# Optimization experiments

Measured on AMD Instinct MI355X. Metric: run time of the kernel, lower is better.

The kernel has to match this reference:

```python
import jax, jax.numpy as jnp
import numpy as np

B, S, D, H = 2, 2048, 1024, 16
DH = D // H
CBS, STRIDE = 32, 16      # compress block size / sliding stride
NSEL = 16                 # num_selected_blocks
WIN = 16                  # sliding_window_size (half-width)
SCALE = DH ** -0.5


def setup_inputs() -> dict:
    key = jax.random.key(0)
    ks = jax.random.split(key, 12)
    s = 0.02
    return {
        "x": jax.random.normal(ks[0], (B, S, D), jnp.float32),
        "qkv_w": jax.random.normal(ks[1], (D, 3 * D), jnp.float32) * s,
        "qkv_b": jnp.zeros((3 * D,), jnp.float32),
        "c1_w": jax.random.normal(ks[2], (CBS * D, D), jnp.float32) * s,
        "c1_b": jnp.zeros((D,), jnp.float32),
        "c2_w": jax.random.normal(ks[3], (D, D), jnp.float32) * s,
        "c2_b": jnp.zeros((D,), jnp.float32),
        "score_w": jax.random.normal(ks[4], (D, 1), jnp.float32) * s,
        "score_b": jnp.zeros((1,), jnp.float32),
        "out_w": jax.random.normal(ks[5], (D, D), jnp.float32) * s,
        "out_b": jnp.zeros((D,), jnp.float32),
    }


def reference(x, qkv_w, qkv_b, c1_w, c1_b, c2_w, c2_b, score_w, score_b, out_w, out_b):
    # q, k, v: [B, H, S, DH]
    qkv = (x @ qkv_w + qkv_b).reshape(B, S, 3, H, DH).transpose(2, 0, 3, 1, 4)
    q, k, v = qkv[0], qkv[1], qkv[2]

    # --- token compression: overlapping blocks -> MLP ---
    starts = jnp.arange(0, S - CBS + 1, STRIDE)                 # [nb]
    blk_idx = starts[:, None] + jnp.arange(CBS)[None, :]        # [nb, CBS]
    blocks = x[:, blk_idx, :].reshape(B, starts.shape[0], CBS * D)
    hidden = jax.nn.relu(blocks @ c1_w + c1_b)
    compressed = hidden @ c2_w + c2_b                           # [B, nb, D]

    # --- block selection via learned scores + top-k ---
    scores = (compressed @ score_w + score_b)[..., 0]           # [B, nb]
    _, top_idx = jax.lax.top_k(scores, NSEL)                    # [B, NSEL]
    selected = jnp.take_along_axis(compressed, top_idx[:, :, None], axis=1)  # [B, NSEL, D]

    sqkv = (selected @ qkv_w + qkv_b).reshape(B, NSEL, 3, H, DH).transpose(2, 0, 3, 1, 4)
    sel_k, sel_v = sqkv[1], sqkv[2]                             # [B, H, NSEL, DH]

    # --- sliding-window local attention (vectorized gather of banded K/V) ---
    offs = jnp.arange(-WIN, WIN + 1)                            # [2W+1]
    pos = jnp.arange(S)[:, None] + offs[None, :]                # [S, 2W+1]
    valid = (pos >= 0) & (pos < S)
    pos_c = jnp.clip(pos, 0, S - 1)
    kw = k[:, :, pos_c, :]                                      # [B, H, S, 2W+1, DH]
    vw = v[:, :, pos_c, :]
    sc = jnp.einsum('bhsd,bhswd->bhsw', q, kw) * SCALE
    sc = jnp.where(valid[None, None], sc, -jnp.inf)
    local = jnp.einsum('bhsw,bhswd->bhsd', jax.nn.softmax(sc, axis=-1), vw)

    # --- global attention over selected compressed blocks ---
    gsc = jnp.einsum('bhsd,bhkd->bhsk', q, sel_k) * SCALE       # [B, H, S, NSEL]
    glob = jnp.einsum('bhsk,bhkd->bhsd', jax.nn.softmax(gsc, axis=-1), sel_v)

    out = (local + glob).transpose(0, 2, 1, 3).reshape(B, S, D)
    return out @ out_w + out_b
```

## Files before the change

kernel.cpp:

```cpp
#include <hip/hip_runtime.h>
#include <math.h>

#define BB   2
#define SS   2048
#define DD   1024
#define HH   16
#define DH   64
#define CBS  32
#define STRIDEC 16
#define NBLK 127
#define NSEL 16
#define WIN  16
#define NW   33
#define SCALE 0.125f
#define MC   254

typedef _Float16 f16;
typedef __attribute__((ext_vector_type(8))) _Float16 f16x8;
typedef __attribute__((ext_vector_type(4))) _Float16 f16x4;
typedef __attribute__((ext_vector_type(2))) _Float16 h2;
typedef __attribute__((ext_vector_type(4))) float f32x4;

__global__ __launch_bounds__(256) void convert_f16(
    const float* __restrict__ src, f16* __restrict__ dst, int n)
{
    const int i = (blockIdx.x * 256 + threadIdx.x) * 4;
    if (i >= n) return;
    float4 v = *(const float4*)(src + i);
    f16x4 o;
    o[0] = (f16)v.x; o[1] = (f16)v.y; o[2] = (f16)v.z; o[3] = (f16)v.w;
    *(f16x4*)(dst + i) = o;
}

__global__ __launch_bounds__(256) void transpose_conv(
    const float* __restrict__ src, f16* __restrict__ dst, int K, int N)
{
    __shared__ float t[32][33];
    const int n0 = blockIdx.x * 32, k0 = blockIdx.y * 32;
    const int tx = threadIdx.x & 31, ty = threadIdx.x >> 5;
#pragma unroll
    for (int r = 0; r < 32; r += 8)
        t[ty + r][tx] = src[(size_t)(k0 + ty + r) * N + n0 + tx];
    __syncthreads();
#pragma unroll
    for (int r = 0; r < 32; r += 8)
        dst[(size_t)(n0 + ty + r) * K + k0 + tx] = (f16)t[tx][ty + r];
}

template<int OUT16>
__global__ __launch_bounds__(256) void gemm_f16(
    const f16* __restrict__ A, const f16* __restrict__ Bt,
    const float* __restrict__ bias, float* __restrict__ C,
    int M, int N, int K)
{
    constexpr int BK = 64;
    __shared__ f16 As[128 * BK];
    __shared__ f16 Bs[128 * BK];
    const int tid  = threadIdx.x;
    const int wid  = tid >> 6, lane = tid & 63;
    const int bm = blockIdx.y * 128, bn = blockIdx.x * 128;
    const int wm = (wid >> 1) * 64, wn = (wid & 1) * 64;

    const int lrow = lane >> 3;
    const int lk8  = (lane & 7) * 8;

    f32x4 acc[4][4];
#pragma unroll
    for (int i = 0; i < 4; ++i)
#pragma unroll
        for (int j = 0; j < 4; ++j) acc[i][j] = (f32x4){0.f, 0.f, 0.f, 0.f};

    for (int kt = 0; kt < K; kt += BK) {
#pragma unroll
        for (int c = 0; c < 4; ++c) {
            const int seg = c * 4 + wid;
            const int row = seg * 8 + lrow;
            const f16* ga = A + (size_t)(bm + row) * K + kt + lk8;
            __builtin_amdgcn_global_load_lds(
                (const __attribute__((address_space(1))) void*)(const void*)ga,
                (__attribute__((address_space(3))) void*)(void*)(As + seg * 512),
                16, 0, 0);
            const f16* gb = Bt + (size_t)(bn + row) * K + kt + lk8;
            __builtin_amdgcn_global_load_lds(
                (const __attribute__((address_space(1))) void*)(const void*)gb,
                (__attribute__((address_space(3))) void*)(void*)(Bs + seg * 512),
                16, 0, 0);
        }
        __syncthreads();

#pragma unroll
        for (int kk = 0; kk < 2; ++kk) {
            const int ko = kk * 32 + (lane >> 4) * 8;
            f16x8 a[4], b[4];
#pragma unroll
            for (int i = 0; i < 4; ++i)
                a[i] = *(const f16x8*)(As + (wm + i * 16 + (lane & 15)) * BK + ko);
#pragma unroll
            for (int j = 0; j < 4; ++j)
                b[j] = *(const f16x8*)(Bs + (wn + j * 16 + (lane & 15)) * BK + ko);
#pragma unroll
            for (int i = 0; i < 4; ++i)
#pragma unroll
                for (int j = 0; j < 4; ++j)
                    acc[i][j] = __builtin_amdgcn_mfma_f32_16x16x32_f16(
                        a[i], b[j], acc[i][j], 0, 0, 0);
        }
        __syncthreads();
    }

    const int rr0 = (lane >> 4) * 4;
    const int cc  = lane & 15;
#pragma unroll
    for (int i = 0; i < 4; ++i) {
        const int r = bm + wm + i * 16 + rr0;
#pragma unroll
        for (int j = 0; j < 4; ++j) {
            const int cn = bn + wn + j * 16 + cc;
            const float bv = bias[cn];
#pragma unroll
            for (int q = 0; q < 4; ++q) {
                if constexpr (OUT16)
                    ((f16*)C)[(size_t)(r + q) * N + cn] = (f16)(acc[i][j][q] + bv);
                else
                    C[(size_t)(r + q) * N + cn] = acc[i][j][q] + bv;
            }
        }
    }
}

#define C1_NZ 16
#define C1_KCHUNK 2048

__global__ __launch_bounds__(256) void gemm_c1(
    const f16* __restrict__ xh, const float* __restrict__ c1w,
    float* __restrict__ P)
{
    constexpr int BK = 64;
    constexpr int BSTR = 72;
    __shared__ f16 As[128 * BK];
    __shared__ f16 Bs[64 * BSTR];
    const int tid  = threadIdx.x;
    const int wid  = tid >> 6, lane = tid & 63;
    const int bn = blockIdx.x * 64, bm = blockIdx.y * 128;
    const int z  = blockIdx.z;
    const int wm = (wid >> 1) * 64, wn = (wid & 1) * 32;

    const int lrow = lane >> 3;
    const int lk8  = (lane & 7) * 8;

    f32x4 acc[4][2];
#pragma unroll
    for (int i = 0; i < 4; ++i)
#pragma unroll
        for (int j = 0; j < 2; ++j) acc[i][j] = (f32x4){0.f, 0.f, 0.f, 0.f};

    for (int t = 0; t < C1_KCHUNK / BK; ++t) {
        const int ktg = z * C1_KCHUNK + t * BK;
        const int kc  = (ktg + lk8) >> 10;
        const int kd  = (ktg + lk8) & 1023;
#pragma unroll
        for (int c = 0; c < 4; ++c) {
            const int seg = c * 4 + wid;
            int row = bm + seg * 8 + lrow;
            if (row > MC - 1) row = MC - 1;
            const int b   = (row >= NBLK) ? 1 : 0;
            const int blk = row - b * NBLK;
            const f16* ga = xh + ((size_t)(b * SS + blk * STRIDEC + kc) << 10) + kd;
            __builtin_amdgcn_global_load_lds(
                (const __attribute__((address_space(1))) void*)(const void*)ga,
                (__attribute__((address_space(3))) void*)(void*)(As + seg * 512),
                16, 0, 0);
        }
        {
            const int kk0 = (tid >> 4) * 2;
            const int n4  = (tid & 15) * 4;
#pragma unroll
            for (int p = 0; p < 2; ++p) {
                const int kk = kk0 + p * 32;
                const float* gB = c1w + (size_t)(ktg + kk) * DD + bn + n4;
                float4 r0 = *(const float4*)gB;
                float4 r1 = *(const float4*)(gB + DD);
                const float a0[4] = {r0.x, r0.y, r0.z, r0.w};
                const float a1[4] = {r1.x, r1.y, r1.z, r1.w};
#pragma unroll
                for (int u = 0; u < 4; ++u) {
                    const int n = n4 + u;
                    h2 w; w[0] = (f16)a0[u]; w[1] = (f16)a1[u];
                    *(h2*)&Bs[n * BSTR + (kk ^ (((n >> 3) & 3) << 3))] = w;
                }
            }
        }
        __syncthreads();

#pragma unroll
        for (int kk = 0; kk < 2; ++kk) {
            const int ko = kk * 32 + (lane >> 4) * 8;
            f16x8 a[4], b[2];
#pragma unroll
            for (int i = 0; i < 4; ++i)
                a[i] = *(const f16x8*)(As + (wm + i * 16 + (lane & 15)) * BK + ko);
#pragma unroll
            for (int j = 0; j < 2; ++j) {
                const int n = wn + j * 16 + (lane & 15);
                b[j] = *(const f16x8*)&Bs[n * BSTR + (ko ^ (((n >> 3) & 3) << 3))];
            }
#pragma unroll
            for (int i = 0; i < 4; ++i)
#pragma unroll
                for (int j = 0; j < 2; ++j)
                    acc[i][j] = __builtin_amdgcn_mfma_f32_16x16x32_f16(
                        a[i], b[j], acc[i][j], 0, 0, 0);
        }
        __syncthreads();
    }

    const int rr0 = (lane >> 4) * 4;
    const int cc  = lane & 15;
#pragma unroll
    for (int i = 0; i < 4; ++i) {
        const int r = bm + wm + i * 16 + rr0;
#pragma unroll
        for (int j = 0; j < 2; ++j) {
            const int cn = bn + wn + j * 16 + cc;
#pragma unroll
            for (int q = 0; q < 4; ++q)
                if (r + q < MC)
                    P[((size_t)z * MC + r + q) * DD + cn] = acc[i][j][q];
        }
    }
}

template<int MODE>
__global__ __launch_bounds__(256) void gemm128(
    const float* __restrict__ A, const float* __restrict__ Bm,
    const float* __restrict__ bias, float* __restrict__ C,
    int M, int N, int K, const int* __restrict__ selIdx, int flags)
{
    __shared__ float As[8][132];
    __shared__ float Bs[8][132];

    const int tid = threadIdx.x;
    const int bm = blockIdx.y * 128;
    const int bn = blockIdx.x * 128;
    const int nz = gridDim.z;
    const int z  = blockIdx.z;
    const int kchunk = K / nz;
    const int k0 = z * kchunk;
    const int kend = k0 + kchunk;

    const int tx = tid & 15;
    const int ty = tid >> 4;

    const int arow = tid >> 1;
    const int akq  = (tid & 1) * 4;
    const int bkr  = tid >> 5;
    const int bcol = (tid & 31) * 4;

    float acc[2][2][4][4];
#pragma unroll
    for (int qi = 0; qi < 2; ++qi)
#pragma unroll
        for (int qj = 0; qj < 2; ++qj)
#pragma unroll
            for (int i = 0; i < 4; ++i)
#pragma unroll
                for (int j = 0; j < 4; ++j) acc[qi][qj][i][j] = 0.f;

    auto loadA = [&](int kt) -> float4 {
        float4 av = make_float4(0.f, 0.f, 0.f, 0.f);
        const int grow = bm + arow;
        if (grow < M) {
            if constexpr (MODE == 0) {
                av = *(const float4*)(A + (size_t)grow * K + kt + akq);
            } else {
                const int b = grow >> 4;
                const int j = grow & 15;
                const int idx = selIdx[b * NSEL + j];
                av = *(const float4*)(A + (size_t)(b * NBLK + idx) * K + kt + akq);
            }
        }
        return av;
    };
    auto loadB = [&](int kt) -> float4 {
        return *(const float4*)(Bm + (size_t)(kt + bkr) * N + bn + bcol);
    };

    float4 av = loadA(k0);
    float4 bv = loadB(k0);

    for (int kt = k0; kt < kend; kt += 8) {
        As[akq + 0][arow] = av.x;
        As[akq + 1][arow] = av.y;
        As[akq + 2][arow] = av.z;
        As[akq + 3][arow] = av.w;
        *(float4*)&Bs[bkr][bcol] = bv;
        __syncthreads();
        if (kt + 8 < kend) {
            av = loadA(kt + 8);
            bv = loadB(kt + 8);
        }
#pragma unroll
        for (int k = 0; k < 8; ++k) {
            const float4 a0 = *(const float4*)&As[k][ty * 4];
            const float4 a1 = *(const float4*)&As[k][64 + ty * 4];
            const float4 b0 = *(const float4*)&Bs[k][tx * 4];
            const float4 b1 = *(const float4*)&Bs[k][64 + tx * 4];
            const float ar[2][4] = {{a0.x, a0.y, a0.z, a0.w},
                                    {a1.x, a1.y, a1.z, a1.w}};
            const float br[2][4] = {{b0.x, b0.y, b0.z, b0.w},
                                    {b1.x, b1.y, b1.z, b1.w}};
#pragma unroll
            for (int qi = 0; qi < 2; ++qi)
#pragma unroll
                for (int i = 0; i < 4; ++i)
#pragma unroll
                    for (int qj = 0; qj < 2; ++qj)
#pragma unroll
                        for (int j = 0; j < 4; ++j)
                            acc[qi][qj][i][j] += ar[qi][i] * br[qj][j];
        }
        __syncthreads();
    }

    if (nz == 1) {
        const bool hasB   = (flags & 1) != 0;
        const bool doRelu = (flags & 2) != 0;
#pragma unroll
        for (int qi = 0; qi < 2; ++qi)
#pragma unroll
            for (int i = 0; i < 4; ++i) {
                const int r = bm + qi * 64 + ty * 4 + i;
                if (r >= M) continue;
#pragma unroll
                for (int qj = 0; qj < 2; ++qj)
#pragma unroll
                    for (int j = 0; j < 4; ++j) {
                        const int cn = bn + qj * 64 + tx * 4 + j;
                        float v = acc[qi][qj][i][j];
                        if (hasB) v += bias[cn];
                        if (doRelu) v = fmaxf(v, 0.f);
                        C[(size_t)r * N + cn] = v;
                    }
            }
    } else {
        float* P = C + (size_t)z * M * N;
#pragma unroll
        for (int qi = 0; qi < 2; ++qi)
#pragma unroll
            for (int i = 0; i < 4; ++i) {
                const int r = bm + qi * 64 + ty * 4 + i;
                if (r >= M) continue;
#pragma unroll
                for (int qj = 0; qj < 2; ++qj)
#pragma unroll
                    for (int j = 0; j < 4; ++j) {
                        const int cn = bn + qj * 64 + tx * 4 + j;
                        P[(size_t)r * N + cn] = acc[qi][qj][i][j];
                    }
            }
    }
}

__global__ __launch_bounds__(256) void reduce_partials(
    const float* __restrict__ P, const float* __restrict__ bias,
    float* __restrict__ outp, int MN, int N, int nz, int doRelu, int halfOut)
{
    const int i = blockIdx.x * 256 + threadIdx.x;
    if (i >= MN) return;
    float s = 0.f;
    for (int z = 0; z < nz; ++z) s += P[(size_t)z * MN + i];
    s += bias[i % N];
    if (doRelu) s = fmaxf(s, 0.f);
    if (halfOut) ((f16*)outp)[i] = (f16)s;
    else         outp[i] = s;
}

__global__ __launch_bounds__(256) void score_kernel(
    const float* __restrict__ comp, const float* __restrict__ sw,
    const float* __restrict__ sb, float* __restrict__ scores)
{
    const int row = blockIdx.x;
    const float* cp = comp + (size_t)row * DD;
    float s = 0.f;
    for (int k = threadIdx.x; k < DD; k += 256) s += cp[k] * sw[k];
#pragma unroll
    for (int off = 32; off >= 1; off >>= 1) s += __shfl_xor(s, off);
    __shared__ float red[4];
    if ((threadIdx.x & 63) == 0) red[threadIdx.x >> 6] = s;
    __syncthreads();
    if (threadIdx.x == 0) scores[row] = red[0] + red[1] + red[2] + red[3] + sb[0];
}

__global__ __launch_bounds__(128) void topk_kernel(
    const float* __restrict__ scores, int* __restrict__ top)
{
    const int b = blockIdx.x;
    const int t = threadIdx.x;
    __shared__ float sval[128];
    __shared__ float sv2[128];
    __shared__ int   si2[128];
    __shared__ unsigned char used[128];
    sval[t] = (t < NBLK) ? scores[b * NBLK + t] : -INFINITY;
    used[t] = 0;
    __syncthreads();
    for (int j = 0; j < NSEL; ++j) {
        sv2[t] = used[t] ? -INFINITY : sval[t];
        si2[t] = t;
        __syncthreads();
        for (int stp = 64; stp >= 1; stp >>= 1) {
            if (t < stp) {
                if (sv2[t + stp] > sv2[t] ||
                    (sv2[t + stp] == sv2[t] && si2[t + stp] < si2[t])) {
                    sv2[t] = sv2[t + stp];
                    si2[t] = si2[t + stp];
                }
            }
            __syncthreads();
        }
        if (t == 0) { top[b * NSEL + j] = si2[0]; used[si2[0]] = 1; }
        __syncthreads();
    }
}

#define QT 64
#define KROWS 96
#define KST2 72
#define VST 136
#define PST 136

__global__ __launch_bounds__(256) void attn_mfma(
    const f16* __restrict__ qkv, const f16* __restrict__ sqkv,
    f16* __restrict__ attn)
{
    __shared__ f16 Kl[KROWS][KST2];
    __shared__ f16 sKl[NSEL][KST2];
    __shared__ f16 Vt[DH][VST];
    __shared__ f16 Pl[4][16][PST];

    int bid = blockIdx.x;
    bid = (bid & 7) * (gridDim.x >> 3) + (bid >> 3);
    const int t = bid & 31;
    const int h = (bid >> 5) & (HH - 1);
    const int b = bid >> 9;
    const int s0 = t * QT;

    const int tid = threadIdx.x;
    const int wid = tid >> 6, lane = tid & 63;
    const int l15 = lane & 15, lg = lane >> 4;

    for (int i = tid; i < KROWS * 8; i += 256) {
        const int row = i >> 3, c8 = (i & 7) * 8;
        const int pos = s0 - WIN + row;
        f16x8 kv, vv;
#pragma unroll
        for (int u = 0; u < 8; ++u) { kv[u] = (f16)0.f; vv[u] = (f16)0.f; }
        if (pos >= 0 && pos < SS) {
            const f16* base = qkv + (size_t)(b * SS + pos) * (3 * DD) + h * DH + c8;
            kv = *(const f16x8*)(base + DD);
            vv = *(const f16x8*)(base + 2 * DD);
        }
        *(f16x8*)&Kl[row][c8] = kv;
#pragma unroll
        for (int u = 0; u < 8; ++u) Vt[c8 + u][row] = vv[u];
    }
    if (tid < NSEL * 8) {
        const int si = tid >> 3, c8 = (tid & 7) * 8;
        const f16* base = sqkv + (size_t)(b * NSEL + si) * (3 * DD) + h * DH + c8;
        f16x8 kv = *(const f16x8*)(base + DD);
        f16x8 vv = *(const f16x8*)(base + 2 * DD);
        *(f16x8*)&sKl[si][c8] = kv;
#pragma unroll
        for (int u = 0; u < 8; ++u) Vt[c8 + u][96 + si] = vv[u];
    }
    for (int i = tid; i < DH * 16; i += 256)
        Vt[i >> 4][112 + (i & 15)] = (f16)0.f;

    f16x8 qf[2];
    {
        const f16* qp = qkv + (size_t)(b * SS + s0 + wid * 16 + l15) * (3 * DD)
                      + h * DH + lg * 8;
        qf[0] = *(const f16x8*)(qp);
        qf[1] = *(const f16x8*)(qp + 32);
    }
    __syncthreads();

    f32x4 aqk[6], asel;
#pragma unroll
    for (int i = 0; i < 6; ++i) aqk[i] = (f32x4){0.f, 0.f, 0.f, 0.f};
    asel = (f32x4){0.f, 0.f, 0.f, 0.f};
#pragma unroll
    for (int kc = 0; kc < 2; ++kc) {
        const int ko = kc * 32 + lg * 8;
#pragma unroll
        for (int kvb = 0; kvb < 6; ++kvb) {
            f16x8 ka = *(const f16x8*)&Kl[kvb * 16 + l15][ko];
            aqk[kvb] = __builtin_amdgcn_mfma_f32_16x16x32_f16(ka, qf[kc], aqk[kvb], 0, 0, 0);
        }
        f16x8 ks = *(const f16x8*)&sKl[l15][ko];
        asel = __builtin_amdgcn_mfma_f32_16x16x32_f16(ks, qf[kc], asel, 0, 0, 0);
    }

    const int qt_ = wid * 16 + l15;
    float sc[6][4];
    float m = -INFINITY;
#pragma unroll
    for (int kvb = 0; kvb < 6; ++kvb)
#pragma unroll
        for (int r = 0; r < 4; ++r) {
            const int kv  = kvb * 16 + lg * 4 + r;
            const int pos = s0 - WIN + kv;
            const int dlt = kv - qt_;
            const bool ok = (dlt >= 0) & (dlt <= 32) & (pos >= 0) & (pos < SS);
            sc[kvb][r] = ok ? aqk[kvb][r] * SCALE : -INFINITY;
            m = fmaxf(m, sc[kvb][r]);
        }
    m = fmaxf(m, __shfl_xor(m, 16));
    m = fmaxf(m, __shfl_xor(m, 32));
    float sum = 0.f;
#pragma unroll
    for (int kvb = 0; kvb < 6; ++kvb)
#pragma unroll
        for (int r = 0; r < 4; ++r) {
            sc[kvb][r] = __expf(sc[kvb][r] - m);
            sum += sc[kvb][r];
        }
    sum += __shfl_xor(sum, 16);
    sum += __shfl_xor(sum, 32);
    const float inv1 = 1.f / sum;

    float s2[4];
    float m2 = -INFINITY;
#pragma unroll
    for (int r = 0; r < 4; ++r) { s2[r] = asel[r] * SCALE; m2 = fmaxf(m2, s2[r]); }
    m2 = fmaxf(m2, __shfl_xor(m2, 16));
    m2 = fmaxf(m2, __shfl_xor(m2, 32));
    float sum2 = 0.f;
#pragma unroll
    for (int r = 0; r < 4; ++r) { s2[r] = __expf(s2[r] - m2); sum2 += s2[r]; }
    sum2 += __shfl_xor(sum2, 16);
    sum2 += __shfl_xor(sum2, 32);
    const float inv2 = 1.f / sum2;

#pragma unroll
    for (int kvb = 0; kvb < 6; ++kvb) {
        h2 p01, p23;
        p01[0] = (f16)(sc[kvb][0] * inv1); p01[1] = (f16)(sc[kvb][1] * inv1);
        p23[0] = (f16)(sc[kvb][2] * inv1); p23[1] = (f16)(sc[kvb][3] * inv1);
        *(h2*)&Pl[wid][l15][kvb * 16 + lg * 4]     = p01;
        *(h2*)&Pl[wid][l15][kvb * 16 + lg * 4 + 2] = p23;
    }
    {
        h2 g01, g23, z0;
        g01[0] = (f16)(s2[0] * inv2); g01[1] = (f16)(s2[1] * inv2);
        g23[0] = (f16)(s2[2] * inv2); g23[1] = (f16)(s2[3] * inv2);
        z0[0] = (f16)0.f; z0[1] = (f16)0.f;
        *(h2*)&Pl[wid][l15][96 + lg * 4]      = g01;
        *(h2*)&Pl[wid][l15][96 + lg * 4 + 2]  = g23;
        *(h2*)&Pl[wid][l15][112 + lg * 4]     = z0;
        *(h2*)&Pl[wid][l15][112 + lg * 4 + 2] = z0;
    }

    f32x4 ov[4];
#pragma unroll
    for (int i = 0; i < 4; ++i) ov[i] = (f32x4){0.f, 0.f, 0.f, 0.f};
#pragma unroll
    for (int kc = 0; kc < 4; ++kc) {
        const int ko = kc * 32 + lg * 8;
        f16x8 pa = *(const f16x8*)&Pl[wid][l15][ko];
#pragma unroll
        for (int db = 0; db < 4; ++db) {
            f16x8 vb = *(const f16x8*)&Vt[db * 16 + l15][ko];
            ov[db] = __builtin_amdgcn_mfma_f32_16x16x32_f16(pa, vb, ov[db], 0, 0, 0);
        }
    }

    const size_t rbase = (size_t)(b * SS + s0 + wid * 16 + lg * 4);
#pragma unroll
    for (int r = 0; r < 4; ++r) {
        f16* op = attn + (rbase + r) * DD + h * DH + l15;
#pragma unroll
        for (int db = 0; db < 4; ++db)
            op[db * 16] = (f16)ov[db][r];
    }
}

extern "C" void kernel_launch(void* const* d_in, const int* in_sizes, int n_in,
                              void* d_out, int out_size, void* d_ws, size_t ws_size,
                              hipStream_t stream)
{
    const float* x       = (const float*)d_in[0];
    const float* qkv_w   = (const float*)d_in[1];
    const float* qkv_b   = (const float*)d_in[2];
    const float* c1_w    = (const float*)d_in[3];
    const float* c1_b    = (const float*)d_in[4];
    const float* c2_w    = (const float*)d_in[5];
    const float* c2_b    = (const float*)d_in[6];
    const float* score_w = (const float*)d_in[7];
    const float* score_b = (const float*)d_in[8];
    const float* out_w   = (const float*)d_in[9];
    const float* out_b   = (const float*)d_in[10];
    float* out = (float*)d_out;
    float* ws  = (float*)d_ws;

    f16*   xh     = (f16*)ws;
    float* A1     = ws + 2097152;
    f16*   qkvb   = (f16*)A1;
    f16*   attnf  = (f16*)(A1 + 12582912);
    float* A2     = ws + 18874368;
    float* part   = A2;
    f16*   qkv_wT = (f16*)A2;
    f16*   out_wT = (f16*)(A2 + 1572864);
    float* hidden = ws + 23035904;
    float* comp   = hidden + 260096;
    float* scores = comp + 260096;
    int*   topIdx = (int*)(scores + 256);
    float* sqkvb  = scores + 256 + 64;

    const int MROWS = BB * SS;
    const int MSEL  = BB * NSEL;

    convert_f16<<<(MROWS * DD) / (256 * 4), 256, 0, stream>>>(x, xh, MROWS * DD);

    gemm_c1<<<dim3(DD / 64, 2, C1_NZ), 256, 0, stream>>>(xh, c1_w, part);

    reduce_partials<<<(MC * DD) / 256, 256, 0, stream>>>(
        part, c1_b, hidden, MC * DD, DD, C1_NZ, 1, 0);

    gemm128<0><<<dim3(DD / 128, 2, 16), 256, 0, stream>>>(
        hidden, c2_w, nullptr, part, MC, DD, DD, nullptr, 0);

    reduce_partials<<<(MC * DD) / 256, 256, 0, stream>>>(
        part, c2_b, comp, MC * DD, DD, 16, 0, 0);

    score_kernel<<<MC, 256, 0, stream>>>(comp, score_w, score_b, scores);

    topk_kernel<<<BB, 128, 0, stream>>>(scores, topIdx);

    gemm128<2><<<dim3(3 * DD / 128, 1, 16), 256, 0, stream>>>(
        comp, qkv_w, nullptr, part, MSEL, 3 * DD, DD, topIdx, 0);

    reduce_partials<<<(MSEL * 3 * DD + 255) / 256, 256, 0, stream>>>(
        part, qkv_b, sqkvb, MSEL * 3 * DD, 3 * DD, 16, 0, 1);

    transpose_conv<<<dim3(3 * DD / 32, DD / 32), 256, 0, stream>>>(
        qkv_w, qkv_wT, DD, 3 * DD);
    transpose_conv<<<dim3(DD / 32, DD / 32), 256, 0, stream>>>(
        out_w, out_wT, DD, DD);

    gemm_f16<1><<<dim3(3 * DD / 128, MROWS / 128), 256, 0, stream>>>(
        xh, qkv_wT, qkv_b, (float*)qkvb, MROWS, 3 * DD, DD);

    attn_mfma<<<BB * HH * (SS / QT), 256, 0, stream>>>(
        qkvb, (const f16*)sqkvb, attnf);

    gemm_f16<0><<<dim3(DD / 128, MROWS / 128), 256, 0, stream>>>(
        attnf, out_wT, out_b, out, MROWS, DD, DD);
}
```

Before: 220.0 us.

## Fold score projection into c2 weights and compress only selected blocks

Precomputes c2_w @ score_w so block scores come straight from the hidden activations, skipping the full 254x1024x1024 c2 GEMM. After top-k, the c2 projection runs only on the 32 selected rows before the QKV projection. The score bias and c2 bias are dropped from the scores, which leaves top-k ordering unchanged because they are constants added to every score. A grid swizzle is also added to gemm_f16 for better L2 locality.

```diff
diff --git a/kernel.cpp b/kernel.cpp
--- a/kernel.cpp
+++ b/kernel.cpp
@@ -58,7 +58,13 @@
     __shared__ f16 Bs[128 * BK];
     const int tid  = threadIdx.x;
     const int wid  = tid >> 6, lane = tid & 63;
-    const int bm = blockIdx.y * 128, bn = blockIdx.x * 128;
+
+    int lin = blockIdx.y * gridDim.x + blockIdx.x;
+    const int nb = gridDim.x * gridDim.y;
+    lin = (lin & 7) * (nb >> 3) + (lin >> 3);
+    const int bx = lin % gridDim.x, by = lin / gridDim.x;
+
+    const int bm = by * 128, bn = bx * 128;
     const int wm = (wid >> 1) * 64, wn = (wid & 1) * 64;
 
     const int lrow = lane >> 3;
@@ -375,20 +381,36 @@
     else         outp[i] = s;
 }
 
-__global__ __launch_bounds__(256) void score_kernel(
-    const float* __restrict__ comp, const float* __restrict__ sw,
-    const float* __restrict__ sb, float* __restrict__ scores)
-{
-    const int row = blockIdx.x;
-    const float* cp = comp + (size_t)row * DD;
+__global__ __launch_bounds__(256) void w2s_kernel(
+    const float* __restrict__ c2w, const float* __restrict__ sw,
+    float* __restrict__ w2s)
+{
+    const int k = blockIdx.x;
+    const float* rp = c2w + (size_t)k * DD;
     float s = 0.f;
-    for (int k = threadIdx.x; k < DD; k += 256) s += cp[k] * sw[k];
+    for (int n = threadIdx.x; n < DD; n += 256) s += rp[n] * sw[n];
 #pragma unroll
     for (int off = 32; off >= 1; off >>= 1) s += __shfl_xor(s, off);
     __shared__ float red[4];
     if ((threadIdx.x & 63) == 0) red[threadIdx.x >> 6] = s;
     __syncthreads();
-    if (threadIdx.x == 0) scores[row] = red[0] + red[1] + red[2] + red[3] + sb[0];
+    if (threadIdx.x == 0) w2s[k] = red[0] + red[1] + red[2] + red[3];
+}
+
+__global__ __launch_bounds__(256) void score2_kernel(
+    const float* __restrict__ hidden, const float* __restrict__ w2s,
+    float* __restrict__ scores)
+{
+    const int row = blockIdx.x;
+    const float* hp = hidden + (size_t)row * DD;
+    float s = 0.f;
+    for (int k = threadIdx.x; k < DD; k += 256) s += hp[k] * w2s[k];
+#pragma unroll
+    for (int off = 32; off >= 1; off >>= 1) s += __shfl_xor(s, off);
+    __shared__ float red[4];
+    if ((threadIdx.x & 63) == 0) red[threadIdx.x >> 6] = s;
+    __syncthreads();
+    if (threadIdx.x == 0) scores[row] = red[0] + red[1] + red[2] + red[3];
 }
 
 __global__ __launch_bounds__(128) void topk_kernel(
@@ -601,20 +623,22 @@
     const float* out_b   = (const float*)d_in[10];
     float* out = (float*)d_out;
     float* ws  = (float*)d_ws;
-
-    f16*   xh     = (f16*)ws;
-    float* A1     = ws + 2097152;
-    f16*   qkvb   = (f16*)A1;
-    f16*   attnf  = (f16*)(A1 + 12582912);
-    float* A2     = ws + 18874368;
-    float* part   = A2;
-    f16*   qkv_wT = (f16*)A2;
-    f16*   out_wT = (f16*)(A2 + 1572864);
-    float* hidden = ws + 23035904;
-    float* comp   = hidden + 260096;
-    float* scores = comp + 260096;
-    int*   topIdx = (int*)(scores + 256);
-    float* sqkvb  = scores + 256 + 64;
+    (void)score_b;
+
+    f16*   xh      = (f16*)ws;
+    float* A1      = ws + 2097152;
+    f16*   qkvb    = (f16*)A1;
+    f16*   attnf   = (f16*)(A1 + 12582912);
+    float* A2      = ws + 18874368;
+    float* part    = A2;
+    f16*   qkv_wT  = (f16*)A2;
+    f16*   out_wT  = (f16*)(A2 + 1572864);
+    float* hidden  = ws + 23035904;
+    float* scores  = hidden + 260096;
+    int*   topIdx  = (int*)(scores + 256);
+    float* sqkvb   = scores + 256 + 64;
+    float* w2s     = sqkvb + 49152;
+    float* compSel = w2s + 1024;
 
     const int MROWS = BB * SS;
     const int MSEL  = BB * NSEL;
@@ -626,18 +650,20 @@
     reduce_partials<<<(MC * DD) / 256, 256, 0, stream>>>(
         part, c1_b, hidden, MC * DD, DD, C1_NZ, 1, 0);
 
-    gemm128<0><<<dim3(DD / 128, 2, 16), 256, 0, stream>>>(
-        hidden, c2_w, nullptr, part, MC, DD, DD, nullptr, 0);
-
-    reduce_partials<<<(MC * DD) / 256, 256, 0, stream>>>(
-        part, c2_b, comp, MC * DD, DD, 16, 0, 0);
-
-    score_kernel<<<MC, 256, 0, stream>>>(comp, score_w, score_b, scores);
+    w2s_kernel<<<DD, 256, 0, stream>>>(c2_w, score_w, w2s);
+
+    score2_kernel<<<MC, 256, 0, stream>>>(hidden, w2s, scores);
 
     topk_kernel<<<BB, 128, 0, stream>>>(scores, topIdx);
 
-    gemm128<2><<<dim3(3 * DD / 128, 1, 16), 256, 0, stream>>>(
-        comp, qkv_w, nullptr, part, MSEL, 3 * DD, DD, topIdx, 0);
+    gemm128<2><<<dim3(DD / 128, 1, 16), 256, 0, stream>>>(
+        hidden, c2_w, nullptr, part, MSEL, DD, DD, topIdx, 0);
+
+    reduce_partials<<<(MSEL * DD) / 256, 256, 0, stream>>>(
+        part, c2_b, compSel, MSEL * DD, DD, 16, 0, 0);
+
+    gemm128<0><<<dim3(3 * DD / 128, 1, 16), 256, 0, stream>>>(
+        compSel, qkv_w, nullptr, part, MSEL, 3 * DD, DD, nullptr, 0);
 
     reduce_partials<<<(MSEL * 3 * DD + 255) / 256, 256, 0, stream>>>(
         part, qkv_b, sqkvb, MSEL * 3 * DD, 3 * DD, 16, 0, 1);
```

New measurement: 218.5 us. About the same (-0.7%).
